# Performance work log

Measured on AMD Instinct MI355X. Metric: run time of the kernel, lower is better.

Reference implementation:

```python
import jax, jax.numpy as jnp
import numpy as np

D, N_EXP, TOP_K = 2048, 64, 8
B, S = 4, 4096

def setup_inputs() -> dict:
    key = jax.random.key(0)
    k1, k2, k3, k4 = jax.random.split(key, 4)
    hidden_states = jax.random.normal(k1, (B, S, D), dtype=jnp.float32)
    # nn.Linear weights are [out, in]; default init ~ U(-1/sqrt(d), 1/sqrt(d))
    bound = 1.0 / np.sqrt(D)
    W_gate = jax.random.uniform(k2, (N_EXP, D), jnp.float32, -bound, bound)
    W_noise = 0.01 * jax.random.normal(k3, (N_EXP, D), dtype=jnp.float32)
    # training-mode noise (router_step % top_k == 0 path): fixed-seed randn
    noise = jax.random.normal(k4, (B, S, N_EXP), dtype=jnp.float32)
    return {"hidden_states": hidden_states, "W_gate": W_gate,
            "W_noise": W_noise, "noise": noise}

def reference(hidden_states, W_gate, W_noise, noise):
    # logits = h @ W_gate^T  : [B,S,n_exp]
    logits = jnp.einsum('bsd,ed->bse', hidden_states, W_gate)
    scale = jax.nn.softplus(jnp.einsum('bsd,ed->bse', hidden_states, W_noise))
    logits = logits + noise * scale
    gates = jax.nn.softmax(logits, axis=-1)
    vals, inds = jax.lax.top_k(gates, TOP_K)  # sorted desc (torch used sorted=False)
    return vals, inds, gates
```

## Files before the change

### kernel.cpp

```cpp
#include <hip/hip_runtime.h>
#include <math.h>

typedef __attribute__((ext_vector_type(8))) _Float16 half8;
typedef __attribute__((ext_vector_type(4))) float    f32x4;

constexpr int D_DIM = 2048;
constexpr int NEXP  = 64;
constexpr int TOPK  = 8;
constexpr int NTOK  = 16384;
constexpr int TM    = 32;
constexpr int BK    = 128;
constexpr int NCH   = D_DIM / BK;
constexpr int NKS   = D_DIM / 32;
constexpr int OSTR  = 132;
constexpr float WSCALE  = 4096.0f;
constexpr float INV_WSC = 1.0f / 4096.0f;

__device__ __forceinline__ unsigned short f16b(float x) {
    _Float16 h = (_Float16)x;
    return __builtin_bit_cast(unsigned short, h);
}
__device__ __forceinline__ float f16tof(unsigned short b) {
    return (float)__builtin_bit_cast(_Float16, b);
}

__global__ void prep_w(const float* __restrict__ Wg, const float* __restrict__ Wn,
                       unsigned short* __restrict__ wsB)
{
    const int idx = blockIdx.x * blockDim.x + threadIdx.x;
    const int n   = idx >> 8;
    const int K8  = idx & 255;
    const float* src = (n < 64) ? (Wg + (size_t)n * D_DIM)
                                : (Wn + (size_t)(n - 64) * D_DIM);
    float4 a = *reinterpret_cast<const float4*>(src + K8 * 8);
    float4 b = *reinterpret_cast<const float4*>(src + K8 * 8 + 4);

    float v[8] = {a.x, a.y, a.z, a.w, b.x, b.y, b.z, b.w};
    union { unsigned short u[8]; half8 s; } H, L;
#pragma unroll
    for (int j = 0; j < 8; ++j) {
        float xs = v[j] * WSCALE;
        unsigned short h = f16b(xs);
        H.u[j] = h;
        L.u[j] = f16b(xs - f16tof(h));
    }
    const int l = ((K8 & 3) * 16) + (n & 15);
    const size_t base = (size_t)(K8 >> 2) * 8192 + (size_t)(n >> 4) * 1024 + (size_t)l * 8;
    *reinterpret_cast<half8*>(wsB + base)       = H.s;
    *reinterpret_cast<half8*>(wsB + base + 512) = L.s;
}

__global__ __launch_bounds__(512, 4)
void noisy_topk_router(const float* __restrict__ hs,
                       const unsigned short* __restrict__ wsB,
                       const float* __restrict__ nz,
                       float* __restrict__ out)
{
    __shared__ __align__(16) char smem[32768];
    unsigned short* stage  = reinterpret_cast<unsigned short*>(smem);
    float*          logits = reinterpret_cast<float*>(smem);

    const int tid  = threadIdx.x;
    const int lane = tid & 63;
    const int w    = tid >> 6;
    const int mt   = w & 1;
    const int np   = w >> 1;
    const int t0   = blockIdx.x * TM;

    const int j0r = lane >> 4;
    const int mr  = lane & 15;
    const int j4  = (j0r & 1) << 2;

    const int r    = tid >> 4;
    const int q    = tid & 15;
    const int ks_s = q >> 2;
    const int j0s  = q & 3;
    const int ms   = r & 15;
    const int mts  = r >> 4;
    const int fs   = ks_s | ((j0s & 1) << 2);
    const int wroff = (mts * 4 + ks_s) * 512 + (j0s * 16 + (ms ^ fs)) * 8;
    const float* hrow = hs + (size_t)(t0 + r) * D_DIM + q * 8;

    const unsigned short* bbase = wsB + (size_t)np * 2048 + (size_t)lane * 8;

    f32x4 accP0[2], accP1[2], accX0[2], accX1[2];
#pragma unroll
    for (int nt = 0; nt < 2; ++nt) {
        accP0[nt] = (f32x4){0.f, 0.f, 0.f, 0.f};
        accP1[nt] = (f32x4){0.f, 0.f, 0.f, 0.f};
        accX0[nt] = (f32x4){0.f, 0.f, 0.f, 0.f};
        accX1[nt] = (f32x4){0.f, 0.f, 0.f, 0.f};
    }

    half8 bh[2][2], bl[2][2];
#pragma unroll
    for (int s = 0; s < 2; ++s)
#pragma unroll
        for (int nt = 0; nt < 2; ++nt) {
            const unsigned short* bp = bbase + (size_t)s * 8192 + nt * 1024;
            bh[s][nt] = *reinterpret_cast<const half8*>(bp);
            bl[s][nt] = *reinterpret_cast<const half8*>(bp + 512);
        }

    auto cvt_write = [&](float4 a, float4 b, unsigned short* buf) {
        float v[8] = {a.x, a.y, a.z, a.w, b.x, b.y, b.z, b.w};
        union { unsigned short u[8]; half8 s; } H, L;
#pragma unroll
        for (int j = 0; j < 8; ++j) {
            unsigned short h = f16b(v[j]);
            H.u[j] = h;
            L.u[j] = f16b(v[j] - f16tof(h));
        }
        *reinterpret_cast<half8*>(buf + wroff)        = H.s;
        *reinterpret_cast<half8*>(buf + wroff + 4096) = L.s;
    };

    {
        float4 a = *reinterpret_cast<const float4*>(hrow);
        float4 b = *reinterpret_cast<const float4*>(hrow + 4);
        cvt_write(a, b, stage);
    }
    __syncthreads();

    for (int c = 0; c < NCH; ++c) {
        float4 pa, pb;
        if (c + 1 < NCH) {
            pa = *reinterpret_cast<const float4*>(hrow + (c + 1) * BK);
            pb = *reinterpret_cast<const float4*>(hrow + (c + 1) * BK + 4);
        }
        const unsigned short* sb = stage + (c & 1) * 8192;

#pragma unroll
        for (int ks = 0; ks < 4; ++ks) {
            const int kk   = c * 4 + ks;
            const int slot = ks & 1;
            const int off  = (mt * 4 + ks) * 512
                           + (j0r * 16 + (mr ^ (ks | j4))) * 8;
            half8 ahi = *reinterpret_cast<const half8*>(sb + off);
            half8 alo = *reinterpret_cast<const half8*>(sb + off + 4096);
#pragma unroll
            for (int nt = 0; nt < 2; ++nt) {
                if ((ks & 1) == 0)
                    accP0[nt] = __builtin_amdgcn_mfma_f32_16x16x32_f16(ahi, bh[slot][nt], accP0[nt], 0, 0, 0);
                else
                    accP1[nt] = __builtin_amdgcn_mfma_f32_16x16x32_f16(ahi, bh[slot][nt], accP1[nt], 0, 0, 0);
                accX0[nt] = __builtin_amdgcn_mfma_f32_16x16x32_f16(ahi, bl[slot][nt], accX0[nt], 0, 0, 0);
                accX1[nt] = __builtin_amdgcn_mfma_f32_16x16x32_f16(alo, bh[slot][nt], accX1[nt], 0, 0, 0);
            }
            if (ks < 2 || c + 1 < NCH) {
                const unsigned short* bp2 = bbase + (size_t)(kk + 2) * 8192;
#pragma unroll
                for (int nt = 0; nt < 2; ++nt) {
                    bh[slot][nt] = *reinterpret_cast<const half8*>(bp2 + nt * 1024);
                    bl[slot][nt] = *reinterpret_cast<const half8*>(bp2 + nt * 1024 + 512);
                }
            }
        }

        if (c + 1 < NCH)
            cvt_write(pa, pb, stage + ((c + 1) & 1) * 8192);
        __syncthreads();
    }

    {
        const int colb = np * 32 + (lane & 15);
        const int rowb = mt * 16 + (lane >> 4) * 4;
#pragma unroll
        for (int nt = 0; nt < 2; ++nt)
#pragma unroll
            for (int rr = 0; rr < 4; ++rr)
                logits[(rowb + rr) * OSTR + colb + nt * 16] =
                    (accP0[nt][rr] + accP1[nt][rr] + accX0[nt][rr] + accX1[nt][rr]) * INV_WSC;
    }
    __syncthreads();

    float* gout = out + (size_t)NTOK * TOPK * 2;
    for (int tt = 0; tt < 4; ++tt) {
        const int tl  = w * 4 + tt;
        const int tok = t0 + tl;
        float gsc = logits[tl * OSTR + lane];
        float nl  = logits[tl * OSTR + 64 + lane];
        float nzv = nz[(size_t)tok * NEXP + lane];
        float sp  = fmaxf(nl, 0.0f) + log1pf(expf(-fabsf(nl)));
        float le  = fmaf(nzv, sp, gsc);

        float mx = le;
#pragma unroll
        for (int d = 32; d > 0; d >>= 1) mx = fmaxf(mx, __shfl_xor(mx, d));
        float pe = expf(le - mx);
        float s  = pe;
#pragma unroll
        for (int d = 32; d > 0; d >>= 1) s += __shfl_xor(s, d);
        float g = pe * (1.0f / s);

        gout[(size_t)tok * NEXP + lane] = g;

        float v = g;
        float keepv = 0.0f;
        int   keepi = 0;
#pragma unroll
        for (int it = 0; it < TOPK; ++it) {
            float m  = v;
            int   mi = lane;
#pragma unroll
            for (int d = 32; d > 0; d >>= 1) {
                float om = __shfl_xor(m, d);
                int   oi = __shfl_xor(mi, d);
                bool take = (om > m) || (om == m && oi < mi);
                m  = take ? om : m;
                mi = take ? oi : mi;
            }
            if (lane == it) { keepv = m; keepi = mi; }
            if (lane == mi) v = -1.0f;
        }
        if (lane < TOPK) {
            out[(size_t)tok * TOPK + lane] = keepv;
            out[(size_t)NTOK * TOPK + (size_t)tok * TOPK + lane] = (float)keepi;
        }
    }
}

extern "C" void kernel_launch(void* const* d_in, const int* in_sizes, int n_in,
                              void* d_out, int out_size, void* d_ws, size_t ws_size,
                              hipStream_t stream) {
    const float* hs = (const float*)d_in[0];
    const float* Wg = (const float*)d_in[1];
    const float* Wn = (const float*)d_in[2];
    const float* nz = (const float*)d_in[3];
    float* out = (float*)d_out;
    unsigned short* wsB = (unsigned short*)d_ws;

    prep_w<<<64, 512, 0, stream>>>(Wg, Wn, wsB);
    noisy_topk_router<<<NTOK / TM, 512, 0, stream>>>(hs, wsB, nz, out);
}
```

Measured before the change: 233.4 us.

## Shrink token tile to 16 and give each wave one 16-expert column slice

```diff
diff --git a/kernel.cpp b/kernel.cpp
--- a/kernel.cpp
+++ b/kernel.cpp
@@ -8,10 +8,9 @@
 constexpr int NEXP  = 64;
 constexpr int TOPK  = 8;
 constexpr int NTOK  = 16384;
-constexpr int TM    = 32;
-constexpr int BK    = 128;
+constexpr int TM    = 16;
+constexpr int BK    = 256;
 constexpr int NCH   = D_DIM / BK;
-constexpr int NKS   = D_DIM / 32;
 constexpr int OSTR  = 132;
 constexpr float WSCALE  = 4096.0f;
 constexpr float INV_WSC = 1.0f / 4096.0f;
@@ -50,7 +49,7 @@
     *reinterpret_cast<half8*>(wsB + base + 512) = L.s;
 }
 
-__global__ __launch_bounds__(512, 4)
+__global__ __launch_bounds__(512, 8)
 void noisy_topk_router(const float* __restrict__ hs,
                        const unsigned short* __restrict__ wsB,
                        const float* __restrict__ nz,
@@ -63,44 +62,33 @@
     const int tid  = threadIdx.x;
     const int lane = tid & 63;
     const int w    = tid >> 6;
-    const int mt   = w & 1;
-    const int np   = w >> 1;
     const int t0   = blockIdx.x * TM;
 
     const int j0r = lane >> 4;
     const int mr  = lane & 15;
-    const int j4  = (j0r & 1) << 2;
-
-    const int r    = tid >> 4;
-    const int q    = tid & 15;
+
+    const int r    = tid >> 5;
+    const int q    = tid & 31;
     const int ks_s = q >> 2;
     const int j0s  = q & 3;
-    const int ms   = r & 15;
-    const int mts  = r >> 4;
-    const int fs   = ks_s | ((j0s & 1) << 2);
-    const int wroff = (mts * 4 + ks_s) * 512 + (j0s * 16 + (ms ^ fs)) * 8;
+    const int fs   = (ks_s & 3) | ((j0s & 1) << 2);
+    const int wroff = ks_s * 512 + (j0s * 16 + (r ^ fs)) * 8;
     const float* hrow = hs + (size_t)(t0 + r) * D_DIM + q * 8;
 
-    const unsigned short* bbase = wsB + (size_t)np * 2048 + (size_t)lane * 8;
-
-    f32x4 accP0[2], accP1[2], accX0[2], accX1[2];
-#pragma unroll
-    for (int nt = 0; nt < 2; ++nt) {
-        accP0[nt] = (f32x4){0.f, 0.f, 0.f, 0.f};
-        accP1[nt] = (f32x4){0.f, 0.f, 0.f, 0.f};
-        accX0[nt] = (f32x4){0.f, 0.f, 0.f, 0.f};
-        accX1[nt] = (f32x4){0.f, 0.f, 0.f, 0.f};
-    }
-
-    half8 bh[2][2], bl[2][2];
-#pragma unroll
-    for (int s = 0; s < 2; ++s)
-#pragma unroll
-        for (int nt = 0; nt < 2; ++nt) {
-            const unsigned short* bp = bbase + (size_t)s * 8192 + nt * 1024;
-            bh[s][nt] = *reinterpret_cast<const half8*>(bp);
-            bl[s][nt] = *reinterpret_cast<const half8*>(bp + 512);
-        }
+    const unsigned short* bbase = wsB + (size_t)w * 1024 + (size_t)lane * 8;
+
+    f32x4 accP0 = (f32x4){0.f, 0.f, 0.f, 0.f};
+    f32x4 accP1 = (f32x4){0.f, 0.f, 0.f, 0.f};
+    f32x4 accX0 = (f32x4){0.f, 0.f, 0.f, 0.f};
+    f32x4 accX1 = (f32x4){0.f, 0.f, 0.f, 0.f};
+
+    half8 bh[2], bl[2];
+#pragma unroll
+    for (int s = 0; s < 2; ++s) {
+        const unsigned short* bp = bbase + (size_t)s * 8192;
+        bh[s] = *reinterpret_cast<const half8*>(bp);
+        bl[s] = *reinterpret_cast<const half8*>(bp + 512);
+    }
 
     auto cvt_write = [&](float4 a, float4 b, unsigned short* buf) {
         float v[8] = {a.x, a.y, a.z, a.w, b.x, b.y, b.z, b.w};
@@ -131,29 +119,23 @@
         const unsigned short* sb = stage + (c & 1) * 8192;
 
 #pragma unroll
-        for (int ks = 0; ks < 4; ++ks) {
-            const int kk   = c * 4 + ks;
+        for (int ks = 0; ks < 8; ++ks) {
+            const int kk   = c * 8 + ks;
             const int slot = ks & 1;
-            const int off  = (mt * 4 + ks) * 512
-                           + (j0r * 16 + (mr ^ (ks | j4))) * 8;
+            const int fr   = (ks & 3) | ((j0r & 1) << 2);
+            const int off  = ks * 512 + (j0r * 16 + (mr ^ fr)) * 8;
             half8 ahi = *reinterpret_cast<const half8*>(sb + off);
             half8 alo = *reinterpret_cast<const half8*>(sb + off + 4096);
-#pragma unroll
-            for (int nt = 0; nt < 2; ++nt) {
-                if ((ks & 1) == 0)
-                    accP0[nt] = __builtin_amdgcn_mfma_f32_16x16x32_f16(ahi, bh[slot][nt], accP0[nt], 0, 0, 0);
-                else
-                    accP1[nt] = __builtin_amdgcn_mfma_f32_16x16x32_f16(ahi, bh[slot][nt], accP1[nt], 0, 0, 0);
-                accX0[nt] = __builtin_amdgcn_mfma_f32_16x16x32_f16(ahi, bl[slot][nt], accX0[nt], 0, 0, 0);
-                accX1[nt] = __builtin_amdgcn_mfma_f32_16x16x32_f16(alo, bh[slot][nt], accX1[nt], 0, 0, 0);
-            }
-            if (ks < 2 || c + 1 < NCH) {
+            if ((ks & 1) == 0)
+                accP0 = __builtin_amdgcn_mfma_f32_16x16x32_f16(ahi, bh[slot], accP0, 0, 0, 0);
+            else
+                accP1 = __builtin_amdgcn_mfma_f32_16x16x32_f16(ahi, bh[slot], accP1, 0, 0, 0);
+            accX0 = __builtin_amdgcn_mfma_f32_16x16x32_f16(ahi, bl[slot], accX0, 0, 0, 0);
+            accX1 = __builtin_amdgcn_mfma_f32_16x16x32_f16(alo, bh[slot], accX1, 0, 0, 0);
+            if (kk + 2 < 64) {
                 const unsigned short* bp2 = bbase + (size_t)(kk + 2) * 8192;
-#pragma unroll
-                for (int nt = 0; nt < 2; ++nt) {
-                    bh[slot][nt] = *reinterpret_cast<const half8*>(bp2 + nt * 1024);
-                    bl[slot][nt] = *reinterpret_cast<const half8*>(bp2 + nt * 1024 + 512);
-                }
+                bh[slot] = *reinterpret_cast<const half8*>(bp2);
+                bl[slot] = *reinterpret_cast<const half8*>(bp2 + 512);
             }
         }
 
@@ -163,20 +145,18 @@
     }
 
     {
-        const int colb = np * 32 + (lane & 15);
-        const int rowb = mt * 16 + (lane >> 4) * 4;
-#pragma unroll
-        for (int nt = 0; nt < 2; ++nt)
-#pragma unroll
-            for (int rr = 0; rr < 4; ++rr)
-                logits[(rowb + rr) * OSTR + colb + nt * 16] =
-                    (accP0[nt][rr] + accP1[nt][rr] + accX0[nt][rr] + accX1[nt][rr]) * INV_WSC;
+        const int colb = w * 16 + mr;
+        const int rowb = j0r * 4;
+#pragma unroll
+        for (int rr = 0; rr < 4; ++rr)
+            logits[(rowb + rr) * OSTR + colb] =
+                (accP0[rr] + accP1[rr] + accX0[rr] + accX1[rr]) * INV_WSC;
     }
     __syncthreads();
 
     float* gout = out + (size_t)NTOK * TOPK * 2;
-    for (int tt = 0; tt < 4; ++tt) {
-        const int tl  = w * 4 + tt;
+    for (int tt = 0; tt < 2; ++tt) {
+        const int tl  = w * 2 + tt;
         const int tok = t0 + tl;
         float gsc = logits[tl * OSTR + lane];
         float nl  = logits[tl * OSTR + 64 + lane];
```

New measurement: 237.2 us. Within noise of the previous version (+1.6%).

## Assign each wave one 16-column N tile across both M tiles, batch B loads per chunk

Applied to the files above, without the earlier changes.

```diff
diff --git a/kernel.cpp b/kernel.cpp
--- a/kernel.cpp
+++ b/kernel.cpp
@@ -11,7 +11,6 @@
 constexpr int TM    = 32;
 constexpr int BK    = 128;
 constexpr int NCH   = D_DIM / BK;
-constexpr int NKS   = D_DIM / 32;
 constexpr int OSTR  = 132;
 constexpr float WSCALE  = 4096.0f;
 constexpr float INV_WSC = 1.0f / 4096.0f;
@@ -63,13 +62,10 @@
     const int tid  = threadIdx.x;
     const int lane = tid & 63;
     const int w    = tid >> 6;
-    const int mt   = w & 1;
-    const int np   = w >> 1;
     const int t0   = blockIdx.x * TM;
 
     const int j0r = lane >> 4;
     const int mr  = lane & 15;
-    const int j4  = (j0r & 1) << 2;
 
     const int r    = tid >> 4;
     const int q    = tid & 15;
@@ -81,26 +77,16 @@
     const int wroff = (mts * 4 + ks_s) * 512 + (j0s * 16 + (ms ^ fs)) * 8;
     const float* hrow = hs + (size_t)(t0 + r) * D_DIM + q * 8;
 
-    const unsigned short* bbase = wsB + (size_t)np * 2048 + (size_t)lane * 8;
+    const unsigned short* bbase = wsB + (size_t)w * 1024 + (size_t)lane * 8;
 
     f32x4 accP0[2], accP1[2], accX0[2], accX1[2];
 #pragma unroll
-    for (int nt = 0; nt < 2; ++nt) {
-        accP0[nt] = (f32x4){0.f, 0.f, 0.f, 0.f};
-        accP1[nt] = (f32x4){0.f, 0.f, 0.f, 0.f};
-        accX0[nt] = (f32x4){0.f, 0.f, 0.f, 0.f};
-        accX1[nt] = (f32x4){0.f, 0.f, 0.f, 0.f};
-    }
-
-    half8 bh[2][2], bl[2][2];
-#pragma unroll
-    for (int s = 0; s < 2; ++s)
-#pragma unroll
-        for (int nt = 0; nt < 2; ++nt) {
-            const unsigned short* bp = bbase + (size_t)s * 8192 + nt * 1024;
-            bh[s][nt] = *reinterpret_cast<const half8*>(bp);
-            bl[s][nt] = *reinterpret_cast<const half8*>(bp + 512);
-        }
+    for (int mt = 0; mt < 2; ++mt) {
+        accP0[mt] = (f32x4){0.f, 0.f, 0.f, 0.f};
+        accP1[mt] = (f32x4){0.f, 0.f, 0.f, 0.f};
+        accX0[mt] = (f32x4){0.f, 0.f, 0.f, 0.f};
+        accX1[mt] = (f32x4){0.f, 0.f, 0.f, 0.f};
+    }
 
     auto cvt_write = [&](float4 a, float4 b, unsigned short* buf) {
         float v[8] = {a.x, a.y, a.z, a.w, b.x, b.y, b.z, b.w};
@@ -122,38 +108,39 @@
     }
     __syncthreads();
 
+#pragma unroll 1
     for (int c = 0; c < NCH; ++c) {
+        half8 bh[4], bl[4];
+#pragma unroll
+        for (int ks = 0; ks < 4; ++ks) {
+            const unsigned short* bp = bbase + (size_t)(c * 4 + ks) * 8192;
+            bh[ks] = *reinterpret_cast<const half8*>(bp);
+            bl[ks] = *reinterpret_cast<const half8*>(bp + 512);
+        }
+        __builtin_amdgcn_sched_barrier(0);
+
         float4 pa, pb;
         if (c + 1 < NCH) {
             pa = *reinterpret_cast<const float4*>(hrow + (c + 1) * BK);
             pb = *reinterpret_cast<const float4*>(hrow + (c + 1) * BK + 4);
         }
+        __builtin_amdgcn_sched_barrier(0);
+
         const unsigned short* sb = stage + (c & 1) * 8192;
-
 #pragma unroll
         for (int ks = 0; ks < 4; ++ks) {
-            const int kk   = c * 4 + ks;
-            const int slot = ks & 1;
-            const int off  = (mt * 4 + ks) * 512
-                           + (j0r * 16 + (mr ^ (ks | j4))) * 8;
-            half8 ahi = *reinterpret_cast<const half8*>(sb + off);
-            half8 alo = *reinterpret_cast<const half8*>(sb + off + 4096);
-#pragma unroll
-            for (int nt = 0; nt < 2; ++nt) {
+            const int fr = ks | ((j0r & 1) << 2);
+#pragma unroll
+            for (int mt = 0; mt < 2; ++mt) {
+                const int off = (mt * 4 + ks) * 512 + (j0r * 16 + (mr ^ fr)) * 8;
+                half8 ahi = *reinterpret_cast<const half8*>(sb + off);
+                half8 alo = *reinterpret_cast<const half8*>(sb + off + 4096);
                 if ((ks & 1) == 0)
-                    accP0[nt] = __builtin_amdgcn_mfma_f32_16x16x32_f16(ahi, bh[slot][nt], accP0[nt], 0, 0, 0);
+                    accP0[mt] = __builtin_amdgcn_mfma_f32_16x16x32_f16(ahi, bh[ks], accP0[mt], 0, 0, 0);
                 else
-                    accP1[nt] = __builtin_amdgcn_mfma_f32_16x16x32_f16(ahi, bh[slot][nt], accP1[nt], 0, 0, 0);
-                accX0[nt] = __builtin_amdgcn_mfma_f32_16x16x32_f16(ahi, bl[slot][nt], accX0[nt], 0, 0, 0);
-                accX1[nt] = __builtin_amdgcn_mfma_f32_16x16x32_f16(alo, bh[slot][nt], accX1[nt], 0, 0, 0);
-            }
-            if (ks < 2 || c + 1 < NCH) {
-                const unsigned short* bp2 = bbase + (size_t)(kk + 2) * 8192;
-#pragma unroll
-                for (int nt = 0; nt < 2; ++nt) {
-                    bh[slot][nt] = *reinterpret_cast<const half8*>(bp2 + nt * 1024);
-                    bl[slot][nt] = *reinterpret_cast<const half8*>(bp2 + nt * 1024 + 512);
-                }
+                    accP1[mt] = __builtin_amdgcn_mfma_f32_16x16x32_f16(ahi, bh[ks], accP1[mt], 0, 0, 0);
+                accX0[mt] = __builtin_amdgcn_mfma_f32_16x16x32_f16(ahi, bl[ks], accX0[mt], 0, 0, 0);
+                accX1[mt] = __builtin_amdgcn_mfma_f32_16x16x32_f16(alo, bh[ks], accX1[mt], 0, 0, 0);
             }
         }
 
@@ -163,14 +150,15 @@
     }
 
     {
-        const int colb = np * 32 + (lane & 15);
-        const int rowb = mt * 16 + (lane >> 4) * 4;
-#pragma unroll
-        for (int nt = 0; nt < 2; ++nt)
+        const int colb = w * 16 + mr;
+#pragma unroll
+        for (int mt = 0; mt < 2; ++mt) {
+            const int rowb = mt * 16 + j0r * 4;
 #pragma unroll
             for (int rr = 0; rr < 4; ++rr)
-                logits[(rowb + rr) * OSTR + colb + nt * 16] =
-                    (accP0[nt][rr] + accP1[nt][rr] + accX0[nt][rr] + accX1[nt][rr]) * INV_WSC;
+                logits[(rowb + rr) * OSTR + colb] =
+                    (accP0[mt][rr] + accP1[mt][rr] + accX0[mt][rr] + accX1[mt][rr]) * INV_WSC;
+        }
     }
     __syncthreads();
 
```

Result: no change. 229.9 us (-1.5%).
